# Kernel optimization log

Measured on AMD Instinct MI355X. Metric: run time of the kernel, lower is better.

## Reference

```python
import jax, jax.numpy as jnp
import numpy as np

B, T, D, DS, EXP = 1, 2048, 512, 32, 2
EPS = 1e-6


def setup_inputs() -> dict:
    key = jax.random.key(0)
    ks = jax.random.split(key, 16)
    g = lambda k, shape, s: jax.random.normal(k, shape, jnp.float32) * s
    x = jax.random.normal(ks[0], (B, T, D), jnp.float32)
    inv = D ** -0.5
    return {
        "x": x,
        "norm_w": jnp.ones((D,), jnp.float32),
        "W_in": g(ks[1], (D, 2 * D), inv),
        "conv_w": g(ks[2], (D, 1, 4), 0.5),          # depthwise, torch layout (O, I/groups, K)
        "conv_b": g(ks[3], (D,), 0.1),
        "W_dt": g(ks[4], (D, D), 0.01 * inv),
        "b_dt": jnp.full((D,), -8.0, jnp.float32) + g(ks[5], (D,), 0.1),  # Mamba-style small-dt init
        "W_B": g(ks[6], (D, DS), inv),
        "W_C": g(ks[7], (D, DS), inv),
        "W_out": g(ks[8], (D, D), inv),
        "log_A": jnp.log(jnp.linspace(1.0, 16.0, D)).astype(jnp.float32),
        "D_param": jnp.ones((D,), jnp.float32),
        "W_ffn1": g(ks[9], (D, EXP * D), inv),
        "W_ffn2": g(ks[10], (EXP * D, D), (EXP * D) ** -0.5),
        "W_merge": g(ks[11], (2 * D, D), (2 * D) ** -0.5),
    }


def _ssm_scan(xs, dt, Bm, Cm, A):
    # cumsum-based parallel scan, exactly as ParallelSSMScan.forward
    log_a = jnp.clip(dt * A[None, None, :], -20.0, 20.0)      # [B,T,D]
    cum = jnp.cumsum(log_a, axis=1)                            # [B,T,D]
    dtx = dt * xs                                              # [B,T,D]
    inp = dtx[..., None] * Bm[:, :, None, :]                   # [B,T,D,ds]
    scaled = jnp.exp(-cum)[..., None] * inp                    # [B,T,D,ds]
    prefix = jnp.cumsum(scaled, axis=1)                        # [B,T,D,ds]
    h_all = jnp.exp(cum)[..., None] * prefix                   # [B,T,D,ds]
    return jnp.einsum('btds,bts->btd', h_all, Cm)


def _forward(x, norm_w, W_in, conv_w, conv_b, W_dt, b_dt, W_B, W_C, W_out,
             log_A, D_param, W_ffn1, W_ffn2, W_merge):
    r = x
    rms = jnp.sqrt(jnp.mean(x * x, axis=-1, keepdims=True) + EPS)
    xn = x / rms * norm_w
    xz = xn @ W_in
    xs, z = jnp.split(xz, 2, axis=-1)
    # causal depthwise conv (padding=3 then [:T] == left-pad 3, valid)
    xt = jnp.transpose(xs, (0, 2, 1))                          # [B,D,T]
    c = jax.lax.conv_general_dilated(
        xt, conv_w, window_strides=(1,), padding=[(3, 0)],
        feature_group_count=D, dimension_numbers=('NCH', 'OIH', 'NCH'))
    c = c + conv_b[None, :, None]
    xs = jax.nn.silu(jnp.transpose(c, (0, 2, 1)))              # [B,T,D]
    dt = jax.nn.softplus(xs @ W_dt + b_dt)
    Bm = xs @ W_B
    Cm = xs @ W_C
    A = -jnp.exp(log_A)
    y = _ssm_scan(xs, dt, Bm, Cm, A)
    y_ssm = (y + xs * D_param) * jax.nn.silu(z)
    y_ssm = y_ssm @ W_out
    y_ffn = jax.nn.gelu(xn @ W_ffn1, approximate=False) @ W_ffn2
    y = jnp.concatenate([y_ssm, y_ffn], axis=-1) @ W_merge
    # dropout in eval mode -> identity
    return r + y


def reference(x, norm_w, W_in, conv_w, conv_b, W_dt, b_dt, W_B, W_C, W_out,
              log_A, D_param, W_ffn1, W_ffn2, W_merge):
    return _forward(x, norm_w, W_in, conv_w, conv_b, W_dt, b_dt, W_B, W_C,
                    W_out, log_A, D_param, W_ffn1, W_ffn2, W_merge)
```

## Files before the change

### kernel.cpp

```cpp
#include <hip/hip_runtime.h>
#include <math.h>

#define T_LEN 2048
#define D_DIM 512
#define NCHUNK 64
#define CLEN 32

typedef __bf16 bf16x8 __attribute__((ext_vector_type(8)));
typedef float f32x4 __attribute__((ext_vector_type(4)));

typedef const __attribute__((address_space(1))) void gvoid;
typedef __attribute__((address_space(3))) void lvoid;

__device__ __forceinline__ void async16(const void* g, void* l) {
  __builtin_amdgcn_global_load_lds((gvoid*)g, (lvoid*)l, 16, 0, 0);
}

__device__ __forceinline__ float silu_f(float x) { return x / (1.f + __expf(-x)); }
__device__ __forceinline__ float softplus_f(float x) {
  return fmaxf(x, 0.f) + log1pf(__expf(-fabsf(x)));
}
__device__ __forceinline__ float gelu_f(float x) {
  return 0.5f * x * (1.f + erff(x * 0.70710678118654752440f));
}
__device__ __forceinline__ unsigned short f2bf(float f) {
  union { float f; unsigned u; } v; v.f = f;
  unsigned r = v.u + 0x7FFF + ((v.u >> 16) & 1);
  return (unsigned short)(r >> 16);
}

struct TransJobs {
  const float* src[8];
  unsigned short* dst[8];
  int K[8];
  int N[8];
  int tr[8];
  int b0[9];
};

__global__ __launch_bounds__(256) void prep_rms_kernel(
    TransJobs J, const float* __restrict__ x, const float* __restrict__ nw,
    unsigned short* __restrict__ xn) {
  const int b = blockIdx.x;
  if (b >= J.b0[8]) {
    const int t = b - J.b0[8];
    const float2 v = reinterpret_cast<const float2*>(x + (size_t)t * D_DIM)[threadIdx.x];
    float ss = v.x * v.x + v.y * v.y;
#pragma unroll
    for (int m = 1; m < 64; m <<= 1) ss += __shfl_xor(ss, m);
    __shared__ float wsum[4];
    if ((threadIdx.x & 63) == 0) wsum[threadIdx.x >> 6] = ss;
    __syncthreads();
    const float tot = wsum[0] + wsum[1] + wsum[2] + wsum[3];
    const float scale = rsqrtf(tot * (1.f / D_DIM) + 1e-6f);
    const float2 wv = reinterpret_cast<const float2*>(nw)[threadIdx.x];
    ushort2 o;
    o.x = f2bf(v.x * scale * wv.x);
    o.y = f2bf(v.y * scale * wv.y);
    reinterpret_cast<ushort2*>(xn + (size_t)t * D_DIM)[threadIdx.x] = o;
    return;
  }
  __shared__ float tile[32][33];
  int ji = 0;
#pragma unroll
  for (int i = 1; i < 8; ++i) ji += (b >= J.b0[i]) ? 1 : 0;
  const float* __restrict__ src = J.src[ji];
  unsigned short* __restrict__ dst = J.dst[ji];
  const int K = J.K[ji], N = J.N[ji];
  const int rel = b - J.b0[ji];
  const int nbx = N >> 5;
  const int bx = rel % nbx, by = rel / nbx;
  const int k0 = by * 32, n0 = bx * 32;
  const int i = threadIdx.x & 31;
  const int r = threadIdx.x >> 5;
  if (J.tr[ji]) {
#pragma unroll
    for (int p = 0; p < 4; ++p) {
      const int kk = r + p * 8;
      tile[kk][i] = src[(size_t)(k0 + kk) * N + n0 + i];
    }
    __syncthreads();
#pragma unroll
    for (int p = 0; p < 4; ++p) {
      const int nn = r + p * 8;
      dst[(size_t)(n0 + nn) * K + k0 + i] = f2bf(tile[i][nn]);
    }
  } else {
#pragma unroll
    for (int p = 0; p < 4; ++p) {
      const int kk = r + p * 8;
      dst[(size_t)(k0 + kk) * N + n0 + i] = f2bf(src[(size_t)(k0 + kk) * N + n0 + i]);
    }
  }
}

__device__ __forceinline__ void gemm64_core(
    const unsigned short* __restrict__ Abf, const unsigned short* __restrict__ Btbf,
    int nt, int lda8, int ldb8, int brow, int bcol,
    bf16x8* __restrict__ As, bf16x8* __restrict__ Bs, f32x4 acc[2][2]) {
  const int tid = threadIdx.x;
  const int lane = tid & 63;
  const int w = tid >> 6;
  const int wrow = (w >> 1) * 32;
  const int wcol = (w & 1) * 32;
  const bf16x8* __restrict__ A8 = reinterpret_cast<const bf16x8*>(Abf);
  const bf16x8* __restrict__ B8 = reinterpret_cast<const bf16x8*>(Btbf);

  const int lr = lane >> 3;
  const int ls = (lane & 7) ^ lr;
  const int wb = w * 64;
  const size_t a0 = (size_t)(brow + w * 8 + lr) * lda8 + ls;
  const size_t a1 = (size_t)(brow + 32 + w * 8 + lr) * lda8 + ls;
  const size_t b0 = (size_t)(bcol + w * 8 + lr) * ldb8 + ls;
  const size_t b1 = (size_t)(bcol + 32 + w * 8 + lr) * ldb8 + ls;

  async16(A8 + a0, As + wb);
  async16(A8 + a1, As + 256 + wb);
  async16(B8 + b0, Bs + wb);
  async16(B8 + b1, Bs + 256 + wb);
  __syncthreads();

  int cur = 0;
  for (int t = 0; t < nt; ++t) {
    if (t + 1 < nt) {
      const int kb = (t + 1) * 8;
      const int nx = (cur ^ 1) * 512;
      async16(A8 + a0 + kb, As + nx + wb);
      async16(A8 + a1 + kb, As + nx + 256 + wb);
      async16(B8 + b0 + kb, Bs + nx + wb);
      async16(B8 + b1 + kb, Bs + nx + 256 + wb);
    }
    const bf16x8* __restrict__ Ac = As + cur * 512;
    const bf16x8* __restrict__ Bc = Bs + cur * 512;
#pragma unroll
    for (int kk = 0; kk < 2; ++kk) {
      const int slot = kk * 4 + (lane >> 4);
      bf16x8 af[2], bf_[2];
#pragma unroll
      for (int m = 0; m < 2; ++m) {
        const int r = wrow + m * 16 + (lane & 15);
        af[m] = Ac[r * 8 + (slot ^ (r & 7))];
      }
#pragma unroll
      for (int n = 0; n < 2; ++n) {
        const int r = wcol + n * 16 + (lane & 15);
        bf_[n] = Bc[r * 8 + (slot ^ (r & 7))];
      }
#pragma unroll
      for (int m = 0; m < 2; ++m)
#pragma unroll
        for (int n = 0; n < 2; ++n)
          acc[m][n] = __builtin_amdgcn_mfma_f32_16x16x32_bf16(af[m], bf_[n], acc[m][n], 0, 0, 0);
    }
    __syncthreads();
    cur ^= 1;
  }
}

__global__ __launch_bounds__(256) void gemm_in_combine(
    const unsigned short* __restrict__ xn_bf, const unsigned short* __restrict__ WinF1T,
    float* __restrict__ xz, unsigned short* __restrict__ comb,
    const unsigned short* __restrict__ WmT, const unsigned short* __restrict__ WoutBF,
    const unsigned short* __restrict__ Wf2BF, unsigned short* __restrict__ WcombT) {
  __shared__ bf16x8 As[1024];
  __shared__ bf16x8 Bs[1024];
  f32x4 acc[2][2];
#pragma unroll
  for (int m = 0; m < 2; ++m)
#pragma unroll
    for (int n = 0; n < 2; ++n) acc[m][n] = {0.f, 0.f, 0.f, 0.f};

  const int b = blockIdx.x;
  const int lane = threadIdx.x & 63;
  const int w = threadIdx.x >> 6;
  const int wrow = (w >> 1) * 32;
  const int wcol = (w & 1) * 32;

  if (b < 1024) {
    const int brow = (b >> 5) * 64;
    const int bcol = (b & 31) * 64;
    gemm64_core(xn_bf, WinF1T, 8, 64, 64, brow, bcol, As, Bs, acc);
#pragma unroll
    for (int m = 0; m < 2; ++m) {
#pragma unroll
      for (int n = 0; n < 2; ++n) {
        const int col = bcol + wcol + n * 16 + (lane & 15);
#pragma unroll
        for (int j = 0; j < 4; ++j) {
          const int row = brow + wrow + m * 16 + (lane >> 4) * 4 + j;
          const float v = acc[m][n][j];
          if (col < 1024) {
            xz[(size_t)row * 1024 + col] = v;
          } else {
            comb[(size_t)row * 1536 + 512 + (col - 1024)] = f2bf(gelu_f(v));
          }
        }
      }
    }
  } else if (b < 1088) {
    const int rel = b - 1024;
    const int brow = (rel >> 3) * 64;
    const int bcol = (rel & 7) * 64;
    gemm64_core(WmT, WoutBF, 8, 128, 64, brow, bcol, As, Bs, acc);
#pragma unroll
    for (int m = 0; m < 2; ++m) {
#pragma unroll
      for (int n = 0; n < 2; ++n) {
        const int col = bcol + wcol + n * 16 + (lane & 15);
#pragma unroll
        for (int j = 0; j < 4; ++j) {
          const int row = brow + wrow + m * 16 + (lane >> 4) * 4 + j;
          WcombT[(size_t)row * 1536 + col] = f2bf(acc[m][n][j]);
        }
      }
    }
  } else {
    const int rel = b - 1088;
    const int brow = (rel >> 4) * 64;
    const int bcol = (rel & 15) * 64;
    gemm64_core(WmT + 512, Wf2BF, 8, 128, 64, brow, bcol, As, Bs, acc);
#pragma unroll
    for (int m = 0; m < 2; ++m) {
#pragma unroll
      for (int n = 0; n < 2; ++n) {
        const int col = bcol + wcol + n * 16 + (lane & 15);
#pragma unroll
        for (int j = 0; j < 4; ++j) {
          const int row = brow + wrow + m * 16 + (lane >> 4) * 4 + j;
          WcombT[(size_t)row * 1536 + 512 + col] = f2bf(acc[m][n][j]);
        }
      }
    }
  }
}

__global__ __launch_bounds__(256) void gemm64_dtbc(
    const unsigned short* __restrict__ Abf, const unsigned short* __restrict__ Btbf,
    float* __restrict__ dt, float* __restrict__ Bm, float* __restrict__ Cm,
    const float* __restrict__ bias) {
  __shared__ bf16x8 As[1024];
  __shared__ bf16x8 Bs[1024];
  f32x4 acc[2][2];
#pragma unroll
  for (int m = 0; m < 2; ++m)
#pragma unroll
    for (int n = 0; n < 2; ++n) acc[m][n] = {0.f, 0.f, 0.f, 0.f};
  const int brow = blockIdx.y * 64;
  const int bcol = blockIdx.x * 64;
  gemm64_core(Abf, Btbf, 8, 64, 64, brow, bcol, As, Bs, acc);

  const int lane = threadIdx.x & 63;
  const int w = threadIdx.x >> 6;
  const int wrow = (w >> 1) * 32;
  const int wcol = (w & 1) * 32;
#pragma unroll
  for (int m = 0; m < 2; ++m) {
#pragma unroll
    for (int n = 0; n < 2; ++n) {
      const int col = bcol + wcol + n * 16 + (lane & 15);
#pragma unroll
      for (int j = 0; j < 4; ++j) {
        const int row = brow + wrow + m * 16 + (lane >> 4) * 4 + j;
        const float v = acc[m][n][j];
        if (col < 512) {
          dt[(size_t)row * 512 + col] = softplus_f(v + bias[col]);
        } else {
          const int s = col - 512;
          float* p = (s < 32) ? Bm : Cm;
          p[(size_t)row * 32 + (s & 31)] = v;
        }
      }
    }
  }
}

__global__ __launch_bounds__(256) void gemm64_merge(
    const unsigned short* __restrict__ Abf, const unsigned short* __restrict__ Btbf,
    float* __restrict__ out, const float* __restrict__ resid) {
  __shared__ bf16x8 As[1024];
  __shared__ bf16x8 Bs[1024];
  f32x4 acc[2][2];
#pragma unroll
  for (int m = 0; m < 2; ++m)
#pragma unroll
    for (int n = 0; n < 2; ++n) acc[m][n] = {0.f, 0.f, 0.f, 0.f};
  const int brow = blockIdx.y * 64;
  const int bcol = blockIdx.x * 64;
  gemm64_core(Abf, Btbf, 24, 192, 192, brow, bcol, As, Bs, acc);

  const int lane = threadIdx.x & 63;
  const int w = threadIdx.x >> 6;
  const int wrow = (w >> 1) * 32;
  const int wcol = (w & 1) * 32;
#pragma unroll
  for (int m = 0; m < 2; ++m) {
#pragma unroll
    for (int n = 0; n < 2; ++n) {
      const int col = bcol + wcol + n * 16 + (lane & 15);
#pragma unroll
      for (int j = 0; j < 4; ++j) {
        const int row = brow + wrow + m * 16 + (lane >> 4) * 4 + j;
        out[(size_t)row * 512 + col] = resid[(size_t)row * 512 + col] + acc[m][n][j];
      }
    }
  }
}

__global__ __launch_bounds__(256) void conv_silu_kernel(
    const float* __restrict__ xz, const float* __restrict__ cw,
    const float* __restrict__ cb, float* __restrict__ xs,
    unsigned short* __restrict__ xs_bf) {
  const int idx = blockIdx.x * 256 + threadIdx.x;
  const int t = idx >> 9;
  const int d = idx & 511;
  const float4 w = reinterpret_cast<const float4*>(cw)[d];
  float acc = cb[d];
  const float wk[4] = {w.x, w.y, w.z, w.w};
#pragma unroll
  for (int k = 0; k < 4; ++k) {
    const int tt = t - 3 + k;
    if (tt >= 0) acc = fmaf(xz[(size_t)tt * 1024 + d], wk[k], acc);
  }
  const float s = silu_f(acc);
  xs[idx] = s;
  xs_bf[idx] = f2bf(s);
}

__global__ __launch_bounds__(256) void prep_gram_kernel(
    const float* __restrict__ dt, const float* __restrict__ xs,
    const float* __restrict__ Bm, const float* __restrict__ Cm,
    const float* __restrict__ log_A,
    unsigned short* __restrict__ U_T, float* __restrict__ E,
    float* __restrict__ V, float* __restrict__ Pc,
    unsigned short* __restrict__ Gm) {
  __shared__ float4 Bls4[CLEN * 8];
  __shared__ float Bls[32][33], Cls[32][33];

  if (blockIdx.x < 128) {
    const int c = blockIdx.x >> 1;
    const int d = (blockIdx.x & 1) * 256 + threadIdx.x;
    Bls4[threadIdx.x] = reinterpret_cast<const float4*>(Bm + c * CLEN * 32)[threadIdx.x];
    __syncthreads();

    const float A = -__expf(log_A[d]);
    float cum = 0.f;
    float e = 1.f;
    float vacc[32];
#pragma unroll
    for (int s = 0; s < 32; ++s) vacc[s] = 0.f;
    unsigned pk[16];
#pragma unroll
    for (int t = 0; t < CLEN; ++t) {
      const int tg = c * CLEN + t;
      const float dtv = dt[(size_t)tg * D_DIM + d];
      const float xv  = xs[(size_t)tg * D_DIM + d];
      const float la = fminf(fmaxf(dtv * A, -20.f), 20.f);
      cum += la;
      e = __expf(cum);
      E[(size_t)tg * D_DIM + d] = e;
      const float u = __expf(-cum) * dtv * xv;
      const unsigned short ub = f2bf(u);
      if ((t & 1) == 0) pk[t >> 1] = (unsigned)ub;
      else              pk[t >> 1] |= ((unsigned)ub) << 16;
#pragma unroll
      for (int s4 = 0; s4 < 8; ++s4) {
        const float4 b = Bls4[t * 8 + s4];
        vacc[s4 * 4 + 0] = fmaf(u, b.x, vacc[s4 * 4 + 0]);
        vacc[s4 * 4 + 1] = fmaf(u, b.y, vacc[s4 * 4 + 1]);
        vacc[s4 * 4 + 2] = fmaf(u, b.z, vacc[s4 * 4 + 2]);
        vacc[s4 * 4 + 3] = fmaf(u, b.w, vacc[s4 * 4 + 3]);
      }
    }
    {
      uint4* dst = reinterpret_cast<uint4*>(U_T + (size_t)d * T_LEN + c * CLEN);
      dst[0] = make_uint4(pk[0], pk[1], pk[2], pk[3]);
      dst[1] = make_uint4(pk[4], pk[5], pk[6], pk[7]);
      dst[2] = make_uint4(pk[8], pk[9], pk[10], pk[11]);
      dst[3] = make_uint4(pk[12], pk[13], pk[14], pk[15]);
    }
    {
      float4* dst = reinterpret_cast<float4*>(V + ((size_t)c * D_DIM + d) * 32);
#pragma unroll
      for (int s4 = 0; s4 < 8; ++s4)
        dst[s4] = make_float4(vacc[s4 * 4], vacc[s4 * 4 + 1], vacc[s4 * 4 + 2], vacc[s4 * 4 + 3]);
    }
    Pc[c * D_DIM + d] = e;
  } else {
    const int c = blockIdx.x - 128;
    {
      const int t = threadIdx.x >> 3;
      const int s4 = threadIdx.x & 7;
      const float4 b = reinterpret_cast<const float4*>(Bm + (c * CLEN + t) * 32)[s4];
      const float4 cc = reinterpret_cast<const float4*>(Cm + (c * CLEN + t) * 32)[s4];
      Bls[t][s4 * 4 + 0] = b.x;  Bls[t][s4 * 4 + 1] = b.y;
      Bls[t][s4 * 4 + 2] = b.z;  Bls[t][s4 * 4 + 3] = b.w;
      Cls[t][s4 * 4 + 0] = cc.x; Cls[t][s4 * 4 + 1] = cc.y;
      Cls[t][s4 * 4 + 2] = cc.z; Cls[t][s4 * 4 + 3] = cc.w;
    }
    __syncthreads();
    const int t = threadIdx.x >> 3;
    const int tp0 = (threadIdx.x & 7) * 4;
    float g[4];
#pragma unroll
    for (int q = 0; q < 4; ++q) {
      const int tp = tp0 + q;
      float acc = 0.f;
      if (tp <= t) {
#pragma unroll
        for (int s = 0; s < 32; ++s) acc = fmaf(Cls[t][s], Bls[tp][s], acc);
      }
      g[q] = acc;
    }
    ushort4 o;
    o.x = f2bf(g[0]); o.y = f2bf(g[1]); o.z = f2bf(g[2]); o.w = f2bf(g[3]);
    reinterpret_cast<ushort4*>(Gm + c * 1024)[threadIdx.x] = o;
  }
}

__global__ __launch_bounds__(256) void state_scan_kernel(
    const float* __restrict__ V, const float* __restrict__ Pc,
    float* __restrict__ Hin) {
  const int gt = blockIdx.x * 256 + threadIdx.x;
  const int d = gt >> 5;
  float h = 0.f;
  for (int c = 0; c < NCHUNK; ++c) {
    Hin[c * 16384 + gt] = h;
    h = Pc[c * D_DIM + d] * (h + V[c * 16384 + gt]);
  }
}

__global__ __launch_bounds__(256) void ssm_out_kernel(
    const unsigned short* __restrict__ Gm, const unsigned short* __restrict__ U_T,
    const float* __restrict__ Hin, const float* __restrict__ Cm,
    const float* __restrict__ E, const float* __restrict__ xs,
    const float* __restrict__ Dp, const float* __restrict__ xz,
    unsigned short* __restrict__ comb) {
  const int c = blockIdx.x;
  const int dt0 = blockIdx.y * 64;
  __shared__ bf16x8 Als[32 * 8];
  __shared__ bf16x8 Bls[64 * 8];
  const int tid = threadIdx.x;

  if (tid < 128) {
    const int t = tid >> 2, q = tid & 3;
    Als[t * 8 + (q ^ (t & 7))] =
        *reinterpret_cast<const bf16x8*>(Gm + c * 1024 + t * 32 + q * 8);
  } else {
    const int i = tid - 128;
    const int t = i >> 2, q = i & 3;
    const float* cp = Cm + (c * CLEN + t) * 32 + q * 8;
    const float4 c0 = *reinterpret_cast<const float4*>(cp);
    const float4 c1 = *reinterpret_cast<const float4*>(cp + 4);
    union { bf16x8 v; unsigned short u[8]; } wv;
    wv.u[0] = f2bf(c0.x); wv.u[1] = f2bf(c0.y); wv.u[2] = f2bf(c0.z); wv.u[3] = f2bf(c0.w);
    wv.u[4] = f2bf(c1.x); wv.u[5] = f2bf(c1.y); wv.u[6] = f2bf(c1.z); wv.u[7] = f2bf(c1.w);
    Als[t * 8 + ((4 + q) ^ (t & 7))] = wv.v;
  }
  {
    const int dd = tid >> 2, q = tid & 3;
    Bls[dd * 8 + (q ^ (dd & 7))] = *reinterpret_cast<const bf16x8*>(
        U_T + (size_t)(dt0 + dd) * T_LEN + c * CLEN + q * 8);
    const float* hp = Hin + ((size_t)c * D_DIM + dt0 + dd) * 32 + q * 8;
    const float4 h0 = *reinterpret_cast<const float4*>(hp);
    const float4 h1 = *reinterpret_cast<const float4*>(hp + 4);
    union { bf16x8 v; unsigned short u[8]; } wv;
    wv.u[0] = f2bf(h0.x); wv.u[1] = f2bf(h0.y); wv.u[2] = f2bf(h0.z); wv.u[3] = f2bf(h0.w);
    wv.u[4] = f2bf(h1.x); wv.u[5] = f2bf(h1.y); wv.u[6] = f2bf(h1.z); wv.u[7] = f2bf(h1.w);
    Bls[dd * 8 + ((4 + q) ^ (dd & 7))] = wv.v;
  }
  __syncthreads();

  const int lane = tid & 63;
  const int w = tid >> 6;
  const int wcol = w * 16;
  f32x4 acc[2];
  acc[0] = {0.f, 0.f, 0.f, 0.f};
  acc[1] = {0.f, 0.f, 0.f, 0.f};
#pragma unroll
  for (int kk = 0; kk < 2; ++kk) {
    const int slot = kk * 4 + (lane >> 4);
    const int rb = wcol + (lane & 15);
    const bf16x8 bfrag = Bls[rb * 8 + (slot ^ (rb & 7))];
#pragma unroll
    for (int m = 0; m < 2; ++m) {
      const int r = m * 16 + (lane & 15);
      const bf16x8 afrag = Als[r * 8 + (slot ^ (r & 7))];
      acc[m] = __builtin_amdgcn_mfma_f32_16x16x32_bf16(afrag, bfrag, acc[m], 0, 0, 0);
    }
  }
  const int dg = dt0 + wcol + (lane & 15);
  const float dpv = Dp[dg];
#pragma unroll
  for (int m = 0; m < 2; ++m) {
#pragma unroll
    for (int j = 0; j < 4; ++j) {
      const int tg = c * CLEN + m * 16 + (lane >> 4) * 4 + j;
      const float y = E[(size_t)tg * D_DIM + dg] * acc[m][j];
      const float xv = xs[(size_t)tg * D_DIM + dg];
      const float zv = xz[(size_t)tg * 1024 + 512 + dg];
      comb[(size_t)tg * 1536 + dg] = f2bf(fmaf(xv, dpv, y) * silu_f(zv));
    }
  }
}

extern "C" void kernel_launch(void* const* d_in, const int* in_sizes, int n_in,
                              void* d_out, int out_size, void* d_ws, size_t ws_size,
                              hipStream_t stream) {
  const float* x      = (const float*)d_in[0];
  const float* norm_w = (const float*)d_in[1];
  const float* W_in   = (const float*)d_in[2];
  const float* conv_w = (const float*)d_in[3];
  const float* conv_b = (const float*)d_in[4];
  const float* W_dt   = (const float*)d_in[5];
  const float* b_dt   = (const float*)d_in[6];
  const float* W_B    = (const float*)d_in[7];
  const float* W_C    = (const float*)d_in[8];
  const float* W_out  = (const float*)d_in[9];
  const float* log_A  = (const float*)d_in[10];
  const float* D_par  = (const float*)d_in[11];
  const float* W_ffn1 = (const float*)d_in[12];
  const float* W_ffn2 = (const float*)d_in[13];
  const float* W_mrg  = (const float*)d_in[14];
  float* out = (float*)d_out;

  const size_t M1 = 1u << 20;
  char* ws = (char*)d_ws;
  size_t off = 0;
  auto alloc_f = [&](size_t n) { float* p = (float*)(ws + off); off += n * 4; return p; };
  auto alloc_h = [&](size_t n) { unsigned short* p = (unsigned short*)(ws + off); off += n * 2; return p; };

  float* xz  = alloc_f(2 * M1);
  float* xs  = alloc_f(M1);
  float* dt  = alloc_f(M1);
  float* E   = alloc_f(M1);
  float* V   = alloc_f(M1);
  float* Hin = alloc_f(M1);
  float* Bm  = alloc_f(1 << 16);
  float* Cm  = alloc_f(1 << 16);
  float* Pc  = alloc_f(NCHUNK * D_DIM);
  unsigned short* U_T    = alloc_h(M1);
  unsigned short* Gm     = alloc_h(NCHUNK * 1024);
  unsigned short* xn_bf  = alloc_h(M1);
  unsigned short* xs_bf  = alloc_h(M1);
  unsigned short* comb   = alloc_h(2048 * 1536);
  unsigned short* WinF1T = alloc_h(2048 * 512);
  unsigned short* WdtBCT = alloc_h(576 * 512);
  unsigned short* WmT    = alloc_h(512 * 1024);
  unsigned short* WoutBF = alloc_h(512 * 512);
  unsigned short* Wf2BF  = alloc_h(1024 * 512);
  unsigned short* WcombT = alloc_h(512 * 1536);

  TransJobs J;
  J.src[0] = W_in;   J.dst[0] = WinF1T;              J.K[0] = 512;  J.N[0] = 1024; J.tr[0] = 1;
  J.src[1] = W_ffn1; J.dst[1] = WinF1T + 1024 * 512; J.K[1] = 512;  J.N[1] = 1024; J.tr[1] = 1;
  J.src[2] = W_dt;   J.dst[2] = WdtBCT;              J.K[2] = 512;  J.N[2] = 512;  J.tr[2] = 1;
  J.src[3] = W_B;    J.dst[3] = WdtBCT + 512 * 512;  J.K[3] = 512;  J.N[3] = 32;   J.tr[3] = 1;
  J.src[4] = W_C;    J.dst[4] = WdtBCT + 544 * 512;  J.K[4] = 512;  J.N[4] = 32;   J.tr[4] = 1;
  J.src[5] = W_mrg;  J.dst[5] = WmT;                 J.K[5] = 1024; J.N[5] = 512;  J.tr[5] = 1;
  J.src[6] = W_out;  J.dst[6] = WoutBF;              J.K[6] = 512;  J.N[6] = 512;  J.tr[6] = 0;
  J.src[7] = W_ffn2; J.dst[7] = Wf2BF;               J.K[7] = 1024; J.N[7] = 512;  J.tr[7] = 0;
  int bacc = 0;
  for (int i = 0; i < 8; ++i) {
    J.b0[i] = bacc;
    bacc += (J.N[i] >> 5) * (J.K[i] >> 5);
  }
  J.b0[8] = bacc;
  prep_rms_kernel<<<bacc + T_LEN, 256, 0, stream>>>(J, x, norm_w, xn_bf);

  gemm_in_combine<<<1216, 256, 0, stream>>>(
      xn_bf, WinF1T, xz, comb, WmT, WoutBF, Wf2BF, WcombT);
  conv_silu_kernel<<<4096, 256, 0, stream>>>(xz, conv_w, conv_b, xs, xs_bf);
  gemm64_dtbc<<<dim3(9, 32), 256, 0, stream>>>(xs_bf, WdtBCT, dt, Bm, Cm, b_dt);
  prep_gram_kernel<<<192, 256, 0, stream>>>(dt, xs, Bm, Cm, log_A, U_T, E, V, Pc, Gm);
  state_scan_kernel<<<64, 256, 0, stream>>>(V, Pc, Hin);
  ssm_out_kernel<<<dim3(NCHUNK, 8), 256, 0, stream>>>(Gm, U_T, Hin, Cm, E, xs, D_par, xz, comb);
  gemm64_merge<<<dim3(8, 32), 256, 0, stream>>>(comb, WcombT, out, x);
}
```

Before: 89.56 us.

## Fuse causal conv and SiLU into the dt/B/C projection GEMM

Removes the separate conv_silu kernel and its bf16 xs buffer. Each dt/B/C GEMM block now computes the depthwise conv and SiLU for its full 64-row by 512 A tile, stores it in swizzled LDS, and streams only the weight tiles double-buffered with async global-to-LDS loads. Only blocks with blockIdx.x == 0 write fp32 xs for later kernels. This saves one launch and a global round trip. In exchange, the conv is recomputed by all 9 column blocks and each block uses 80KB of LDS, which limits occupancy.

```diff
diff --git a/kernel.cpp b/kernel.cpp
--- a/kernel.cpp
+++ b/kernel.cpp
@@ -234,25 +234,118 @@
   }
 }
 
-__global__ __launch_bounds__(256) void gemm64_dtbc(
-    const unsigned short* __restrict__ Abf, const unsigned short* __restrict__ Btbf,
-    float* __restrict__ dt, float* __restrict__ Bm, float* __restrict__ Cm,
-    const float* __restrict__ bias) {
-  __shared__ bf16x8 As[1024];
-  __shared__ bf16x8 Bs[1024];
-  f32x4 acc[2][2];
-#pragma unroll
-  for (int m = 0; m < 2; ++m)
-#pragma unroll
-    for (int n = 0; n < 2; ++n) acc[m][n] = {0.f, 0.f, 0.f, 0.f};
+__global__ __launch_bounds__(256) void conv_dtbc_kernel(
+    const float* __restrict__ xz, const float* __restrict__ cw,
+    const float* __restrict__ cb, const unsigned short* __restrict__ WdtBCT,
+    float* __restrict__ xs, float* __restrict__ dt, float* __restrict__ Bm,
+    float* __restrict__ Cm, const float* __restrict__ bias) {
+  __shared__ bf16x8 XsT[64 * 64];
+  __shared__ bf16x8 Bs[2 * 512];
+  const int tid = threadIdx.x;
+  const int lane = tid & 63;
+  const int w = tid >> 6;
   const int brow = blockIdx.y * 64;
   const int bcol = blockIdx.x * 64;
-  gemm64_core(Abf, Btbf, 8, 64, 64, brow, bcol, As, Bs, acc);
-
-  const int lane = threadIdx.x & 63;
-  const int w = threadIdx.x >> 6;
+
+#pragma unroll
+  for (int p = 0; p < 16; ++p) {
+    const int idx = p * 256 + tid;
+    const int row = idx >> 6;
+    const int slot = idx & 63;
+    const int d0 = slot * 8;
+    const int t = brow + row;
+    float a[8];
+    {
+      const float4 c0 = *reinterpret_cast<const float4*>(cb + d0);
+      const float4 c1 = *reinterpret_cast<const float4*>(cb + d0 + 4);
+      a[0] = c0.x; a[1] = c0.y; a[2] = c0.z; a[3] = c0.w;
+      a[4] = c1.x; a[5] = c1.y; a[6] = c1.z; a[7] = c1.w;
+    }
+    float4 wv[8];
+#pragma unroll
+    for (int i = 0; i < 8; ++i)
+      wv[i] = *reinterpret_cast<const float4*>(cw + (d0 + i) * 4);
+#pragma unroll
+    for (int k = 0; k < 4; ++k) {
+      const int tt = t - 3 + k;
+      if (tt >= 0) {
+        const float4 x0 = *reinterpret_cast<const float4*>(xz + (size_t)tt * 1024 + d0);
+        const float4 x1 = *reinterpret_cast<const float4*>(xz + (size_t)tt * 1024 + d0 + 4);
+        const float xv[8] = {x0.x, x0.y, x0.z, x0.w, x1.x, x1.y, x1.z, x1.w};
+#pragma unroll
+        for (int i = 0; i < 8; ++i) {
+          const float wk = (k == 0) ? wv[i].x : (k == 1) ? wv[i].y
+                         : (k == 2) ? wv[i].z : wv[i].w;
+          a[i] = fmaf(xv[i], wk, a[i]);
+        }
+      }
+    }
+#pragma unroll
+    for (int i = 0; i < 8; ++i) a[i] = silu_f(a[i]);
+    union { bf16x8 v; unsigned u[4]; } pk;
+#pragma unroll
+    for (int j = 0; j < 4; ++j)
+      pk.u[j] = (unsigned)f2bf(a[2 * j]) | ((unsigned)f2bf(a[2 * j + 1]) << 16);
+    XsT[row * 64 + (slot ^ (row & 7))] = pk.v;
+    if (blockIdx.x == 0) {
+      float4* o = reinterpret_cast<float4*>(xs + (size_t)t * 512 + d0);
+      o[0] = make_float4(a[0], a[1], a[2], a[3]);
+      o[1] = make_float4(a[4], a[5], a[6], a[7]);
+    }
+  }
+
+  const bf16x8* __restrict__ B8 = reinterpret_cast<const bf16x8*>(WdtBCT);
+  const int lr = lane >> 3;
+  const int ls = (lane & 7) ^ lr;
+  const int wb = w * 64;
+  const size_t b0 = (size_t)(bcol + w * 8 + lr) * 64 + ls;
+  const size_t b1 = (size_t)(bcol + 32 + w * 8 + lr) * 64 + ls;
+
+  async16(B8 + b0, Bs + wb);
+  async16(B8 + b1, Bs + 256 + wb);
+  __syncthreads();
+
   const int wrow = (w >> 1) * 32;
   const int wcol = (w & 1) * 32;
+  f32x4 acc[2][2];
+#pragma unroll
+  for (int m = 0; m < 2; ++m)
+#pragma unroll
+    for (int n = 0; n < 2; ++n) acc[m][n] = {0.f, 0.f, 0.f, 0.f};
+
+  int cur = 0;
+  for (int t = 0; t < 8; ++t) {
+    if (t + 1 < 8) {
+      const int kb = (t + 1) * 8;
+      const int nx = (cur ^ 1) * 512;
+      async16(B8 + b0 + kb, Bs + nx + wb);
+      async16(B8 + b1 + kb, Bs + nx + 256 + wb);
+    }
+    const bf16x8* __restrict__ Bc = Bs + cur * 512;
+#pragma unroll
+    for (int kk = 0; kk < 2; ++kk) {
+      const int s8 = kk * 4 + (lane >> 4);
+      bf16x8 af[2], bf_[2];
+#pragma unroll
+      for (int m = 0; m < 2; ++m) {
+        const int r = wrow + m * 16 + (lane & 15);
+        af[m] = XsT[r * 64 + t * 8 + (s8 ^ (r & 7))];
+      }
+#pragma unroll
+      for (int n = 0; n < 2; ++n) {
+        const int r = wcol + n * 16 + (lane & 15);
+        bf_[n] = Bc[r * 8 + (s8 ^ (r & 7))];
+      }
+#pragma unroll
+      for (int m = 0; m < 2; ++m)
+#pragma unroll
+        for (int n = 0; n < 2; ++n)
+          acc[m][n] = __builtin_amdgcn_mfma_f32_16x16x32_bf16(af[m], bf_[n], acc[m][n], 0, 0, 0);
+    }
+    __syncthreads();
+    cur ^= 1;
+  }
+
 #pragma unroll
   for (int m = 0; m < 2; ++m) {
 #pragma unroll
@@ -304,26 +397,6 @@
       }
     }
   }
-}
-
-__global__ __launch_bounds__(256) void conv_silu_kernel(
-    const float* __restrict__ xz, const float* __restrict__ cw,
-    const float* __restrict__ cb, float* __restrict__ xs,
-    unsigned short* __restrict__ xs_bf) {
-  const int idx = blockIdx.x * 256 + threadIdx.x;
-  const int t = idx >> 9;
-  const int d = idx & 511;
-  const float4 w = reinterpret_cast<const float4*>(cw)[d];
-  float acc = cb[d];
-  const float wk[4] = {w.x, w.y, w.z, w.w};
-#pragma unroll
-  for (int k = 0; k < 4; ++k) {
-    const int tt = t - 3 + k;
-    if (tt >= 0) acc = fmaf(xz[(size_t)tt * 1024 + d], wk[k], acc);
-  }
-  const float s = silu_f(acc);
-  xs[idx] = s;
-  xs_bf[idx] = f2bf(s);
 }
 
 __global__ __launch_bounds__(256) void prep_gram_kernel(
@@ -541,7 +614,6 @@
   unsigned short* U_T    = alloc_h(M1);
   unsigned short* Gm     = alloc_h(NCHUNK * 1024);
   unsigned short* xn_bf  = alloc_h(M1);
-  unsigned short* xs_bf  = alloc_h(M1);
   unsigned short* comb   = alloc_h(2048 * 1536);
   unsigned short* WinF1T = alloc_h(2048 * 512);
   unsigned short* WdtBCT = alloc_h(576 * 512);
@@ -569,8 +641,8 @@
 
   gemm_in_combine<<<1216, 256, 0, stream>>>(
       xn_bf, WinF1T, xz, comb, WmT, WoutBF, Wf2BF, WcombT);
-  conv_silu_kernel<<<4096, 256, 0, stream>>>(xz, conv_w, conv_b, xs, xs_bf);
-  gemm64_dtbc<<<dim3(9, 32), 256, 0, stream>>>(xs_bf, WdtBCT, dt, Bm, Cm, b_dt);
+  conv_dtbc_kernel<<<dim3(9, 32), 256, 0, stream>>>(
+      xz, conv_w, conv_b, WdtBCT, xs, dt, Bm, Cm, b_dt);
   prep_gram_kernel<<<192, 256, 0, stream>>>(dt, xs, Bm, Cm, log_A, U_T, E, V, Pc, Gm);
   state_scan_kernel<<<64, 256, 0, stream>>>(V, Pc, Hin);
   ssm_out_kernel<<<dim3(NCHUNK, 8), 256, 0, stream>>>(Gm, U_T, Hin, Cm, E, xs, D_par, xz, comb);
```

Measured after the change: 141.5 us. +58.0%, slower.
